# Kernel tuning notes

Hardware: AMD Instinct MI355X
Metric: run time of the kernel (lower is better)

Reference implementation:

```python
import jax, jax.numpy as jnp
import numpy as np

B, S, H = 2, 2048, 2048
INTER = 1024
N_ROUTED = 8
ZERO = 4
TOTAL = N_ROUTED + ZERO
TOP_K = 2
SCALE = 1.5


def setup_inputs() -> dict:
    key = jax.random.key(0)
    k0, k1, k2, k3, k4, k5 = jax.random.split(key, 6)
    w = 0.02  # weight init scale
    return {
        "hidden_states": jax.random.normal(k0, (B, S, H), jnp.float32),
        "classifier_w": jax.random.normal(k1, (TOTAL, H), jnp.float32) * w,
        "e_score_correction_bias": jax.random.normal(k2, (TOTAL,), jnp.float32) * w,
        "gate_w": jax.random.normal(k3, (N_ROUTED, INTER, H), jnp.float32) * w,
        "up_w": jax.random.normal(k4, (N_ROUTED, INTER, H), jnp.float32) * w,
        "down_w": jax.random.normal(k5, (N_ROUTED, H, INTER), jnp.float32) * w,
    }


def reference(hidden_states, classifier_w, e_score_correction_bias, gate_w, up_w, down_w):
    x = hidden_states  # [B,S,H]
    total = classifier_w.shape[0]
    n_routed = gate_w.shape[0]

    # --- Router: softmax over all experts, bias only for selection ---
    logits = jnp.einsum('bsh,eh->bse', x, classifier_w)          # [B,S,total]
    probs = jax.nn.softmax(logits, axis=-1)
    biased = probs + e_score_correction_bias
    _, idx = jax.lax.top_k(biased, TOP_K)                         # [B,S,K] int
    rw = jnp.take_along_axis(probs, idx, axis=-1) * SCALE         # unbiased probs as weights

    # Dense per-expert weight via one-hot combine (Equal+Mul+ReduceSum in original)
    w_full = jnp.sum(jax.nn.one_hot(idx, total, dtype=x.dtype) * rw[..., None], axis=-2)  # [B,S,total]

    # --- Compute ALL routed experts densely (matches original op graph) ---
    g = jnp.einsum('bsh,eih->bsei', x, gate_w)                    # [B,S,E,INTER]
    u = jnp.einsum('bsh,eih->bsei', x, up_w)
    act = jax.nn.silu(g) * u
    expert_out = jnp.einsum('bsei,ehi->bseh', act, down_w)        # [B,S,E,H]

    out = jnp.einsum('bse,bseh->bsh', w_full[..., :n_routed], expert_out)
    # Zero (identity) experts pass hidden_states through
    out = out + x * jnp.sum(w_full[..., n_routed:], axis=-1, keepdims=True)
    return out
```

## Files before the change

kernel.cpp:

```cpp
#include <hip/hip_runtime.h>
#include <cstdint>

#define T_TOKENS 4096
#define HDIM 2048
#define IDIM 1024
#define NEXP 8
#define NTOT 12
#define MAX_SLOTS 8320

typedef __bf16 bf16x8_t __attribute__((ext_vector_type(8)));
typedef float f32x4_t __attribute__((ext_vector_type(4)));
typedef unsigned short u16x8_t __attribute__((ext_vector_type(8)));
typedef unsigned short u16x4_t __attribute__((ext_vector_type(4)));

__device__ __forceinline__ unsigned short f2bf(float f) {
    unsigned int u = __builtin_bit_cast(unsigned int, f);
    u += 0x7fffu + ((u >> 16) & 1u);
    return (unsigned short)(u >> 16);
}
__device__ __forceinline__ float bfu2f(unsigned short u) {
    unsigned int v = ((unsigned int)u) << 16;
    return __builtin_bit_cast(float, v);
}
__device__ __forceinline__ void async16(const unsigned short* g, unsigned short* l) {
    __builtin_amdgcn_global_load_lds(
        (const unsigned int __attribute__((address_space(1)))*)g,
        (unsigned int __attribute__((address_space(3)))*)l,
        16, 0, 0);
}
__device__ __forceinline__ void cvt16(const float* src, unsigned short* dst) {
    f32x4_t f0 = ((const f32x4_t*)src)[0];
    f32x4_t f1 = ((const f32x4_t*)src)[1];
    f32x4_t f2 = ((const f32x4_t*)src)[2];
    f32x4_t f3 = ((const f32x4_t*)src)[3];
    u16x8_t a, b;
#pragma unroll
    for (int j = 0; j < 4; ++j) { a[j] = f2bf(f0[j]); a[4 + j] = f2bf(f1[j]); }
#pragma unroll
    for (int j = 0; j < 4; ++j) { b[j] = f2bf(f2[j]); b[4 + j] = f2bf(f3[j]); }
    ((u16x8_t*)dst)[0] = a;
    ((u16x8_t*)dst)[1] = b;
}

__global__ void init_kernel(int* __restrict__ meta) {
    int i = threadIdx.x;
    if (i < 32) meta[i] = 0;
}

__global__ void noop_kernel() {}

__global__ void pack_w_kernel(const float* __restrict__ gw, const float* __restrict__ uw,
                              const float* __restrict__ dw,
                              unsigned short* __restrict__ guwb,
                              unsigned short* __restrict__ dwb) {
    const int n8_gu = NEXP * 2 * IDIM * HDIM / 8;
    const int n8_d = NEXP * HDIM * IDIM / 8;
    int stride = gridDim.x * blockDim.x;
    for (int i = blockIdx.x * blockDim.x + threadIdx.x; i < n8_gu + n8_d; i += stride) {
        if (i < n8_gu) {
            size_t f = (size_t)i * 8;
            int h = (int)(f & (HDIM - 1));
            int p = (int)((f >> 11) & 2047);
            int e = (int)(f >> 22);
            int j = p >> 5, r = p & 31;
            const float* base = (r < 16) ? gw : uw;
            const float* src = base + ((size_t)e * IDIM + 16 * j + (r & 15)) * HDIM + h;
            f32x4_t a = ((const f32x4_t*)src)[0];
            f32x4_t b = ((const f32x4_t*)src)[1];
            u16x8_t o;
#pragma unroll
            for (int q = 0; q < 4; ++q) { o[q] = f2bf(a[q]); o[4 + q] = f2bf(b[q]); }
            ((u16x8_t*)guwb)[i] = o;
        } else {
            int k = i - n8_gu;
            const f32x4_t* p4 = (const f32x4_t*)(dw + (size_t)k * 8);
            f32x4_t a = p4[0], b = p4[1];
            u16x8_t o;
#pragma unroll
            for (int q = 0; q < 4; ++q) { o[q] = f2bf(a[q]); o[4 + q] = f2bf(b[q]); }
            ((u16x8_t*)dwb)[k] = o;
        }
    }
}

__global__ void router_kernel(const float* __restrict__ x,
                              const float* __restrict__ cw,
                              const float* __restrict__ bias,
                              int* __restrict__ counts,
                              int* __restrict__ tok_e,
                              float* __restrict__ tok_w,
                              float* __restrict__ zero_w,
                              unsigned short* __restrict__ xb) {
    const int token = blockIdx.x;
    const int ln = threadIdx.x;
    const float* xr = x + (size_t)token * HDIM;
    float acc[NTOT];
#pragma unroll
    for (int e = 0; e < NTOT; ++e) acc[e] = 0.f;
    for (int h0 = ln * 4; h0 < HDIM; h0 += 256) {
        f32x4_t xv = *(const f32x4_t*)(xr + h0);
        if (xb) {
            u16x4_t o;
#pragma unroll
            for (int j = 0; j < 4; ++j) o[j] = f2bf(xv[j]);
            *(u16x4_t*)(xb + (size_t)token * HDIM + h0) = o;
        }
#pragma unroll
        for (int e = 0; e < NTOT; ++e) {
            f32x4_t wv = *(const f32x4_t*)(cw + e * HDIM + h0);
            acc[e] += xv[0] * wv[0] + xv[1] * wv[1] + xv[2] * wv[2] + xv[3] * wv[3];
        }
    }
#pragma unroll
    for (int e = 0; e < NTOT; ++e) {
        float v = acc[e];
#pragma unroll
        for (int s = 32; s > 0; s >>= 1) v += __shfl_xor(v, s, 64);
        acc[e] = v;
    }
    if (ln == 0) {
        float mx = acc[0];
#pragma unroll
        for (int e = 1; e < NTOT; ++e) mx = fmaxf(mx, acc[e]);
        float p[NTOT];
        float sum = 0.f;
#pragma unroll
        for (int e = 0; e < NTOT; ++e) { p[e] = __expf(acc[e] - mx); sum += p[e]; }
        float inv = 1.f / sum;
#pragma unroll
        for (int e = 0; e < NTOT; ++e) p[e] *= inv;
        float b[NTOT];
#pragma unroll
        for (int e = 0; e < NTOT; ++e) b[e] = p[e] + bias[e];
        int i0 = 0; float v0 = b[0];
#pragma unroll
        for (int e = 1; e < NTOT; ++e) if (b[e] > v0) { v0 = b[e]; i0 = e; }
        int i1 = -1; float v1 = -3.0e38f;
#pragma unroll
        for (int e = 0; e < NTOT; ++e) if (e != i0 && b[e] > v1) { v1 = b[e]; i1 = e; }
        if (i1 < 0) i1 = (i0 == 0) ? 1 : 0;
        float w0 = p[i0] * 1.5f, w1 = p[i1] * 1.5f;
        tok_e[2 * token] = i0; tok_e[2 * token + 1] = i1;
        tok_w[2 * token] = w0; tok_w[2 * token + 1] = w1;
        float zw = 0.f;
        if (i0 >= NEXP) zw += w0; else atomicAdd(&counts[i0], 1);
        if (i1 >= NEXP) zw += w1; else atomicAdd(&counts[i1], 1);
        zero_w[token] = zw;
    }
}

__global__ void scan_kernel(const int* __restrict__ counts, int* __restrict__ offs) {
    if (threadIdx.x == 0 && blockIdx.x == 0) {
        int a = 0;
        for (int e = 0; e < NEXP; ++e) {
            offs[e] = a;
            int c = counts[e];
            if (c < 0) c = 0;
            if (c > T_TOKENS) c = T_TOKENS;
            a += c;
        }
        if (a > 2 * T_TOKENS) a = 2 * T_TOKENS;
        offs[NEXP] = a;
    }
}

__global__ void place_kernel(const int* __restrict__ tok_e, const float* __restrict__ tok_w,
                             const int* __restrict__ offs, int* __restrict__ fill,
                             int* __restrict__ token_list, float* __restrict__ slot_w,
                             int* __restrict__ map) {
    int token = blockIdx.x * blockDim.x + threadIdx.x;
    if (token >= T_TOKENS) return;
#pragma unroll
    for (int j = 0; j < 2; ++j) {
        int e = tok_e[2 * token + j];
        int m = -1;
        if (e >= 0 && e < NEXP) {
            int pos = atomicAdd(&fill[e], 1);
            int slot = offs[e] + pos;
            if (slot >= 0 && slot < 2 * T_TOKENS) {
                token_list[slot] = token;
                slot_w[slot] = tok_w[2 * token + j];
                m = slot;
            }
        }
        map[2 * token + j] = m;
    }
}

__launch_bounds__(256, 3)
__global__ void gemm1_kernel(const unsigned short* __restrict__ xb,
                             const unsigned short* __restrict__ guwb,
                             const int* __restrict__ offs,
                             const int* __restrict__ token_list,
                             const float* __restrict__ slot_w,
                             unsigned short* __restrict__ act) {
    const int e = blockIdx.z;
    const int off = offs[e];
    int Me = offs[e + 1] - off;
    if (Me < 0) Me = 0;
    if (Me > T_TOKENS) Me = T_TOKENS;
    const int m0 = blockIdx.y * 128;
    if (m0 >= Me) return;
    const int n0 = blockIdx.x * 128;

    __shared__ __align__(16) unsigned short As[128][32];
    __shared__ __align__(16) unsigned short Bs[128][32];

    const int tid = threadIdx.x;
    const int wv = tid >> 6, ln = tid & 63;
    const int sc = (ln & 3) * 8;

    int tr0 = m0 + wv * 16 + (ln >> 2);      if (tr0 >= Me) tr0 = Me - 1;
    int tr1 = m0 + 64 + wv * 16 + (ln >> 2); if (tr1 >= Me) tr1 = Me - 1;
    int tok0 = token_list[off + tr0]; if (tok0 < 0 || tok0 >= T_TOKENS) tok0 = 0;
    int tok1 = token_list[off + tr1]; if (tok1 < 0 || tok1 >= T_TOKENS) tok1 = 0;
    const unsigned short* aA0 = xb + (size_t)tok0 * HDIM + sc;
    const unsigned short* aA1 = xb + (size_t)tok1 * HDIM + sc;
    unsigned short* lA0 = &As[wv * 16][0];
    unsigned short* lA1 = &As[64 + wv * 16][0];

    const unsigned short* aB0 = guwb + (size_t)e * 2 * IDIM * HDIM +
                                (size_t)(n0 + wv * 16 + (ln >> 2)) * HDIM + sc;
    const unsigned short* aB1 = aB0 + (size_t)64 * HDIM;
    unsigned short* lB0 = &Bs[wv * 16][0];
    unsigned short* lB1 = &Bs[64 + wv * 16][0];

    const int wm = wv & 1, wn = wv >> 1;
    const int fr = ln & 15;
    const int fk = (ln >> 4) * 8;

    f32x4_t acc[4][4] = {};

    for (int k0 = 0; k0 < HDIM; k0 += 32) {
        async16(aA0 + k0, lA0);
        async16(aA1 + k0, lA1);
        async16(aB0 + k0, lB0);
        async16(aB1 + k0, lB1);
        __syncthreads();
        bf16x8_t af[4], bfr[4];
#pragma unroll
        for (int t = 0; t < 4; ++t) {
            af[t] = *(const bf16x8_t*)&As[wm * 64 + t * 16 + fr][fk];
            bfr[t] = *(const bf16x8_t*)&Bs[wn * 64 + t * 16 + fr][fk];
        }
#pragma unroll
        for (int mt = 0; mt < 4; ++mt)
#pragma unroll
            for (int nt = 0; nt < 4; ++nt)
                acc[mt][nt] = __builtin_amdgcn_mfma_f32_16x16x32_bf16(af[mt], bfr[nt], acc[mt][nt], 0, 0, 0);
        __syncthreads();
    }

    const int ibase = (n0 >> 1) + wn * 32;
#pragma unroll
    for (int mt = 0; mt < 4; ++mt) {
#pragma unroll
        for (int r = 0; r < 4; ++r) {
            int rloc = wm * 64 + mt * 16 + (ln >> 4) * 4 + r;
            int grow = m0 + rloc;
            if (grow < Me) {
                float w = slot_w[off + grow];
                size_t rb = (size_t)(off + grow) * IDIM + ibase;
#pragma unroll
                for (int t = 0; t < 2; ++t) {
                    float g = acc[mt][2 * t][r];
                    float u = acc[mt][2 * t + 1][r];
                    float s = g / (1.f + __expf(-g));
                    act[rb + t * 16 + fr] = f2bf(s * u * w);
                }
            }
        }
    }
}

__launch_bounds__(256, 3)
__global__ void gemm2_kernel(const unsigned short* __restrict__ act,
                             const unsigned short* __restrict__ dwb,
                             const int* __restrict__ offs,
                             unsigned short* __restrict__ dout) {
    const int e = blockIdx.z;
    const int off = offs[e];
    int Me = offs[e + 1] - off;
    if (Me < 0) Me = 0;
    if (Me > T_TOKENS) Me = T_TOKENS;
    const int m0 = blockIdx.y * 128;
    if (m0 >= Me) return;
    const int n0 = blockIdx.x * 128;

    __shared__ __align__(16) unsigned short As[128][32];
    __shared__ __align__(16) unsigned short Bs[128][32];

    const int tid = threadIdx.x;
    const int wv = tid >> 6, ln = tid & 63;
    const int sc = (ln & 3) * 8;

    const int sr = wv * 16 + (ln >> 2);
    int ar0 = off + m0 + sr;      if (ar0 >= MAX_SLOTS) ar0 = MAX_SLOTS - 1;
    int ar1 = off + m0 + 64 + sr; if (ar1 >= MAX_SLOTS) ar1 = MAX_SLOTS - 1;
    const unsigned short* aA0 = act + (size_t)ar0 * IDIM + sc;
    const unsigned short* aA1 = act + (size_t)ar1 * IDIM + sc;
    unsigned short* lA0 = &As[wv * 16][0];
    unsigned short* lA1 = &As[64 + wv * 16][0];

    const unsigned short* aB0 = dwb + (size_t)e * HDIM * IDIM +
                                (size_t)(n0 + wv * 16 + (ln >> 2)) * IDIM + sc;
    const unsigned short* aB1 = aB0 + (size_t)64 * IDIM;
    unsigned short* lB0 = &Bs[wv * 16][0];
    unsigned short* lB1 = &Bs[64 + wv * 16][0];

    const int wm = wv & 1, wn = wv >> 1;
    const int fr = ln & 15;
    const int fk = (ln >> 4) * 8;

    f32x4_t acc[4][4] = {};

    for (int k0 = 0; k0 < IDIM; k0 += 32) {
        async16(aA0 + k0, lA0);
        async16(aA1 + k0, lA1);
        async16(aB0 + k0, lB0);
        async16(aB1 + k0, lB1);
        __syncthreads();
        bf16x8_t af[4], bfr[4];
#pragma unroll
        for (int t = 0; t < 4; ++t) {
            af[t] = *(const bf16x8_t*)&As[wm * 64 + t * 16 + fr][fk];
            bfr[t] = *(const bf16x8_t*)&Bs[wn * 64 + t * 16 + fr][fk];
        }
#pragma unroll
        for (int mt = 0; mt < 4; ++mt)
#pragma unroll
            for (int nt = 0; nt < 4; ++nt)
                acc[mt][nt] = __builtin_amdgcn_mfma_f32_16x16x32_bf16(af[mt], bfr[nt], acc[mt][nt], 0, 0, 0);
        __syncthreads();
    }

#pragma unroll
    for (int mt = 0; mt < 4; ++mt) {
#pragma unroll
        for (int r = 0; r < 4; ++r) {
            int rloc = wm * 64 + mt * 16 + (ln >> 4) * 4 + r;
            int grow = m0 + rloc;
            if (grow < Me) {
                size_t rb = (size_t)(off + grow) * HDIM + n0;
#pragma unroll
                for (int nt = 0; nt < 4; ++nt)
                    dout[rb + wn * 64 + nt * 16 + fr] = f2bf(acc[mt][nt][r]);
            }
        }
    }
}

__launch_bounds__(256, 2)
__global__ void gemm1_fb(const float* __restrict__ x,
                         const float* __restrict__ gate_w,
                         const float* __restrict__ up_w,
                         const int* __restrict__ offs,
                         const int* __restrict__ token_list,
                         const float* __restrict__ slot_w,
                         unsigned short* __restrict__ act) {
    const int e = blockIdx.z;
    const int off = offs[e];
    int Me = offs[e + 1] - off;
    if (Me < 0) Me = 0;
    if (Me > T_TOKENS) Me = T_TOKENS;
    const int m0 = blockIdx.y * 128;
    if (m0 >= Me) return;
    const int n0 = blockIdx.x * 128;

    __shared__ __align__(16) unsigned short As[128][32];
    __shared__ __align__(16) unsigned short Gs[128][32];
    __shared__ __align__(16) unsigned short Us[128][32];

    const int tid = threadIdx.x;
    const int srow = tid >> 1;
    const int shalf = (tid & 1) * 16;

    int tr = m0 + srow; if (tr >= Me) tr = Me - 1;
    int tok = token_list[off + tr];
    if (tok < 0 || tok >= T_TOKENS) tok = 0;
    const float* aA = x + (size_t)tok * HDIM + shalf;
    const float* aG = gate_w + (size_t)e * IDIM * HDIM + (size_t)(n0 + srow) * HDIM + shalf;
    const float* aU = up_w + (size_t)e * IDIM * HDIM + (size_t)(n0 + srow) * HDIM + shalf;
    unsigned short* lA = &As[srow][shalf];
    unsigned short* lG = &Gs[srow][shalf];
    unsigned short* lU = &Us[srow][shalf];

    const int wv = tid >> 6, ln = tid & 63;
    const int wm = wv & 1, wn = wv >> 1;
    const int fr = ln & 15;
    const int fk = (ln >> 4) * 8;

    f32x4_t accg[4][4] = {};
    f32x4_t accu[4][4] = {};

    for (int k0 = 0; k0 < HDIM; k0 += 32) {
        cvt16(aA + k0, lA);
        cvt16(aG + k0, lG);
        cvt16(aU + k0, lU);
        __syncthreads();
        bf16x8_t af[4], gf[4], uf[4];
#pragma unroll
        for (int t = 0; t < 4; ++t) {
            af[t] = *(const bf16x8_t*)&As[wm * 64 + t * 16 + fr][fk];
            gf[t] = *(const bf16x8_t*)&Gs[wn * 64 + t * 16 + fr][fk];
            uf[t] = *(const bf16x8_t*)&Us[wn * 64 + t * 16 + fr][fk];
        }
#pragma unroll
        for (int mt = 0; mt < 4; ++mt)
#pragma unroll
            for (int nt = 0; nt < 4; ++nt) {
                accg[mt][nt] = __builtin_amdgcn_mfma_f32_16x16x32_bf16(af[mt], gf[nt], accg[mt][nt], 0, 0, 0);
                accu[mt][nt] = __builtin_amdgcn_mfma_f32_16x16x32_bf16(af[mt], uf[nt], accu[mt][nt], 0, 0, 0);
            }
        __syncthreads();
    }

#pragma unroll
    for (int mt = 0; mt < 4; ++mt) {
#pragma unroll
        for (int r = 0; r < 4; ++r) {
            int rloc = wm * 64 + mt * 16 + (ln >> 4) * 4 + r;
            int grow = m0 + rloc;
            if (grow < Me) {
                float w = slot_w[off + grow];
                size_t rb = (size_t)(off + grow) * IDIM + n0;
#pragma unroll
                for (int nt = 0; nt < 4; ++nt) {
                    float g = accg[mt][nt][r];
                    float u = accu[mt][nt][r];
                    float s = g / (1.f + __expf(-g));
                    act[rb + wn * 64 + nt * 16 + fr] = f2bf(s * u * w);
                }
            }
        }
    }
}

__launch_bounds__(256, 2)
__global__ void gemm2_fb(const unsigned short* __restrict__ act,
                         const float* __restrict__ dwn,
                         const int* __restrict__ offs,
                         unsigned short* __restrict__ dout) {
    const int e = blockIdx.z;
    const int off = offs[e];
    int Me = offs[e + 1] - off;
    if (Me < 0) Me = 0;
    if (Me > T_TOKENS) Me = T_TOKENS;
    const int m0 = blockIdx.y * 128;
    if (m0 >= Me) return;
    const int n0 = blockIdx.x * 128;

    __shared__ __align__(16) unsigned short As[128][32];
    __shared__ __align__(16) unsigned short Bs[128][32];

    const int tid = threadIdx.x;
    const int wv = tid >> 6, ln = tid & 63;

    const int sr0 = wv * 16 + (ln >> 2);
    const int sc = (ln & 3) * 8;
    int ar0 = off + m0 + sr0;      if (ar0 >= MAX_SLOTS) ar0 = MAX_SLOTS - 1;
    int ar1 = off + m0 + 64 + sr0; if (ar1 >= MAX_SLOTS) ar1 = MAX_SLOTS - 1;
    const unsigned short* aA0 = act + (size_t)ar0 * IDIM + sc;
    const unsigned short* aA1 = act + (size_t)ar1 * IDIM + sc;
    unsigned short* lA0 = &As[wv * 16][0];
    unsigned short* lA1 = &As[64 + wv * 16][0];

    const int srow = tid >> 1;
    const int shalf = (tid & 1) * 16;
    const float* aB = dwn + (size_t)e * HDIM * IDIM + (size_t)(n0 + srow) * IDIM + shalf;
    unsigned short* lB = &Bs[srow][shalf];

    const int wm = wv & 1, wn = wv >> 1;
    const int fr = ln & 15;
    const int fk = (ln >> 4) * 8;

    f32x4_t acc[4][4] = {};

    for (int k0 = 0; k0 < IDIM; k0 += 32) {
        async16(aA0 + k0, lA0);
        async16(aA1 + k0, lA1);
        cvt16(aB + k0, lB);
        __syncthreads();
        bf16x8_t af[4], bfr[4];
#pragma unroll
        for (int t = 0; t < 4; ++t) {
            af[t] = *(const bf16x8_t*)&As[wm * 64 + t * 16 + fr][fk];
            bfr[t] = *(const bf16x8_t*)&Bs[wn * 64 + t * 16 + fr][fk];
        }
#pragma unroll
        for (int mt = 0; mt < 4; ++mt)
#pragma unroll
            for (int nt = 0; nt < 4; ++nt)
                acc[mt][nt] = __builtin_amdgcn_mfma_f32_16x16x32_bf16(af[mt], bfr[nt], acc[mt][nt], 0, 0, 0);
        __syncthreads();
    }

#pragma unroll
    for (int mt = 0; mt < 4; ++mt) {
#pragma unroll
        for (int r = 0; r < 4; ++r) {
            int rloc = wm * 64 + mt * 16 + (ln >> 4) * 4 + r;
            int grow = m0 + rloc;
            if (grow < Me) {
                size_t rb = (size_t)(off + grow) * HDIM + n0;
#pragma unroll
                for (int nt = 0; nt < 4; ++nt)
                    dout[rb + wn * 64 + nt * 16 + fr] = f2bf(acc[mt][nt][r]);
            }
        }
    }
}

__global__ void finalize_kernel(const float* __restrict__ x,
                                const unsigned short* __restrict__ dout,
                                const int* __restrict__ map,
                                const float* __restrict__ zero_w,
                                float* __restrict__ out) {
    int gid = blockIdx.x * blockDim.x + threadIdx.x;
    int token = gid >> 8;
    int hg = (gid & 255) * 8;
    int s0 = map[2 * token], s1 = map[2 * token + 1];
    float zw = zero_w[token];
    size_t base = (size_t)token * HDIM + hg;
    f32x4_t x0 = *(const f32x4_t*)(x + base);
    f32x4_t x1 = *(const f32x4_t*)(x + base + 4);
    float o[8];
#pragma unroll
    for (int j = 0; j < 4; ++j) { o[j] = zw * x0[j]; o[4 + j] = zw * x1[j]; }
    if (s0 >= 0 && s0 < 2 * T_TOKENS) {
        u16x8_t d = *(const u16x8_t*)(dout + (size_t)s0 * HDIM + hg);
#pragma unroll
        for (int j = 0; j < 8; ++j) o[j] += bfu2f(d[j]);
    }
    if (s1 >= 0 && s1 < 2 * T_TOKENS) {
        u16x8_t d = *(const u16x8_t*)(dout + (size_t)s1 * HDIM + hg);
#pragma unroll
        for (int j = 0; j < 8; ++j) o[j] += bfu2f(d[j]);
    }
    f32x4_t o0, o1;
#pragma unroll
    for (int j = 0; j < 4; ++j) { o0[j] = o[j]; o1[j] = o[4 + j]; }
    *(f32x4_t*)(out + base) = o0;
    *(f32x4_t*)(out + base + 4) = o1;
}

extern "C" void kernel_launch(void* const* d_in, const int* in_sizes, int n_in,
                              void* d_out, int out_size, void* d_ws, size_t ws_size,
                              hipStream_t stream) {
    const float* x = (const float*)d_in[0];
    const float* cw = (const float*)d_in[1];
    const float* bias = (const float*)d_in[2];
    const float* gw = (const float*)d_in[3];
    const float* uw = (const float*)d_in[4];
    const float* dw = (const float*)d_in[5];
    float* out = (float*)d_out;

    char* ws = (char*)d_ws;
    int* counts = (int*)(ws + 0);
    int* fill = (int*)(ws + 32);
    int* offs = (int*)(ws + 64);
    int* tok_e = (int*)(ws + 128);
    float* tok_w = (float*)(ws + 32896);
    float* zero_w = (float*)(ws + 65664);
    int* map = (int*)(ws + 82048);
    int* token_list = (int*)(ws + 114816);
    float* slot_w = (float*)(ws + 148096);
    unsigned short* act = (unsigned short*)(ws + 181504);
    unsigned short* dout = (unsigned short*)(ws + 17220864);
    const size_t needed_small = 51299584ull;
    unsigned short* xb   = (unsigned short*)(ws + 51299584ull);
    unsigned short* guwb = (unsigned short*)(ws + 68076800ull);
    unsigned short* dwb  = (unsigned short*)(ws + 135185664ull);
    const size_t needed_big = 168740096ull;

    if (ws_size < needed_small) {
        noop_kernel<<<1, 64, 0, stream>>>();
        return;
    }

    init_kernel<<<1, 64, 0, stream>>>((int*)ws);

    if (ws_size >= needed_big) {
        router_kernel<<<T_TOKENS, 64, 0, stream>>>(x, cw, bias, counts, tok_e, tok_w, zero_w, xb);
        scan_kernel<<<1, 64, 0, stream>>>(counts, offs);
        place_kernel<<<(T_TOKENS + 255) / 256, 256, 0, stream>>>(tok_e, tok_w, offs, fill,
                                                                 token_list, slot_w, map);
        pack_w_kernel<<<4096, 256, 0, stream>>>(gw, uw, dw, guwb, dwb);
        gemm1_kernel<<<dim3(2 * IDIM / 128, 32, NEXP), 256, 0, stream>>>(xb, guwb, offs,
                                                                         token_list, slot_w, act);
        gemm2_kernel<<<dim3(HDIM / 128, 32, NEXP), 256, 0, stream>>>(act, dwb, offs, dout);
    } else {
        router_kernel<<<T_TOKENS, 64, 0, stream>>>(x, cw, bias, counts, tok_e, tok_w, zero_w,
                                                   (unsigned short*)nullptr);
        scan_kernel<<<1, 64, 0, stream>>>(counts, offs);
        place_kernel<<<(T_TOKENS + 255) / 256, 256, 0, stream>>>(tok_e, tok_w, offs, fill,
                                                                 token_list, slot_w, map);
        gemm1_fb<<<dim3(IDIM / 128, 32, NEXP), 256, 0, stream>>>(x, gw, uw, offs,
                                                                 token_list, slot_w, act);
        gemm2_fb<<<dim3(HDIM / 128, 32, NEXP), 256, 0, stream>>>(act, dw, offs, dout);
    }

    finalize_kernel<<<(T_TOKENS * HDIM / 8 + 255) / 256, 256, 0, stream>>>(x, dout, map,
                                                                           zero_w, out);
}
```

Before: 500.4 us.

## Double-buffer LDS tiles and XOR-swizzle columns in both expert GEMMs

Both grouped GEMM kernels now use two LDS buffers, so the next K-slice is loaded asynchronously while MFMAs run on the current one, which hides global-load latency behind compute. The global source column is XOR-swizzled per row and the fragment read column is swizzled to match, with the aim of reducing LDS bank conflicts on the 16-byte fragment reads. LDS use doubles, which may lower occupancy under launch_bounds(256,3). The single barrier per iteration relies on the async-load wait semantics being correct for the prefetched buffer.

Result: no change. 501.1 us (+0.1%).

```diff
diff --git a/kernel.cpp b/kernel.cpp
--- a/kernel.cpp
+++ b/kernel.cpp
@@ -203,45 +203,53 @@
     if (m0 >= Me) return;
     const int n0 = blockIdx.x * 128;
 
-    __shared__ __align__(16) unsigned short As[128][32];
-    __shared__ __align__(16) unsigned short Bs[128][32];
+    __shared__ __align__(16) unsigned short As[2][128][32];
+    __shared__ __align__(16) unsigned short Bs[2][128][32];
 
     const int tid = threadIdx.x;
     const int wv = tid >> 6, ln = tid & 63;
-    const int sc = (ln & 3) * 8;
-
-    int tr0 = m0 + wv * 16 + (ln >> 2);      if (tr0 >= Me) tr0 = Me - 1;
-    int tr1 = m0 + 64 + wv * 16 + (ln >> 2); if (tr1 >= Me) tr1 = Me - 1;
+    const int R = ln >> 2;
+    const int scs = (((ln & 3) ^ ((R & 3) ^ ((R >> 2) & 1))) * 8);
+
+    int tr0 = m0 + wv * 16 + R;      if (tr0 >= Me) tr0 = Me - 1;
+    int tr1 = m0 + 64 + wv * 16 + R; if (tr1 >= Me) tr1 = Me - 1;
     int tok0 = token_list[off + tr0]; if (tok0 < 0 || tok0 >= T_TOKENS) tok0 = 0;
     int tok1 = token_list[off + tr1]; if (tok1 < 0 || tok1 >= T_TOKENS) tok1 = 0;
-    const unsigned short* aA0 = xb + (size_t)tok0 * HDIM + sc;
-    const unsigned short* aA1 = xb + (size_t)tok1 * HDIM + sc;
-    unsigned short* lA0 = &As[wv * 16][0];
-    unsigned short* lA1 = &As[64 + wv * 16][0];
+    const unsigned short* aA0 = xb + (size_t)tok0 * HDIM + scs;
+    const unsigned short* aA1 = xb + (size_t)tok1 * HDIM + scs;
 
     const unsigned short* aB0 = guwb + (size_t)e * 2 * IDIM * HDIM +
-                                (size_t)(n0 + wv * 16 + (ln >> 2)) * HDIM + sc;
+                                (size_t)(n0 + wv * 16 + R) * HDIM + scs;
     const unsigned short* aB1 = aB0 + (size_t)64 * HDIM;
-    unsigned short* lB0 = &Bs[wv * 16][0];
-    unsigned short* lB1 = &Bs[64 + wv * 16][0];
 
     const int wm = wv & 1, wn = wv >> 1;
     const int fr = ln & 15;
     const int fk = (ln >> 4) * 8;
+    const int fswz = ((fr & 3) ^ ((fr >> 2) & 1)) * 8;
+    const int fcol = fk ^ fswz;
 
     f32x4_t acc[4][4] = {};
 
+    async16(aA0, &As[0][wv * 16][0]);
+    async16(aA1, &As[0][64 + wv * 16][0]);
+    async16(aB0, &Bs[0][wv * 16][0]);
+    async16(aB1, &Bs[0][64 + wv * 16][0]);
+    __syncthreads();
+
+    int cur = 0;
     for (int k0 = 0; k0 < HDIM; k0 += 32) {
-        async16(aA0 + k0, lA0);
-        async16(aA1 + k0, lA1);
-        async16(aB0 + k0, lB0);
-        async16(aB1 + k0, lB1);
-        __syncthreads();
+        const int nxt = cur ^ 1;
+        if (k0 + 32 < HDIM) {
+            async16(aA0 + k0 + 32, &As[nxt][wv * 16][0]);
+            async16(aA1 + k0 + 32, &As[nxt][64 + wv * 16][0]);
+            async16(aB0 + k0 + 32, &Bs[nxt][wv * 16][0]);
+            async16(aB1 + k0 + 32, &Bs[nxt][64 + wv * 16][0]);
+        }
         bf16x8_t af[4], bfr[4];
 #pragma unroll
         for (int t = 0; t < 4; ++t) {
-            af[t] = *(const bf16x8_t*)&As[wm * 64 + t * 16 + fr][fk];
-            bfr[t] = *(const bf16x8_t*)&Bs[wn * 64 + t * 16 + fr][fk];
+            af[t] = *(const bf16x8_t*)&As[cur][wm * 64 + t * 16 + fr][fcol];
+            bfr[t] = *(const bf16x8_t*)&Bs[cur][wn * 64 + t * 16 + fr][fcol];
         }
 #pragma unroll
         for (int mt = 0; mt < 4; ++mt)
@@ -249,6 +257,7 @@
             for (int nt = 0; nt < 4; ++nt)
                 acc[mt][nt] = __builtin_amdgcn_mfma_f32_16x16x32_bf16(af[mt], bfr[nt], acc[mt][nt], 0, 0, 0);
         __syncthreads();
+        cur = nxt;
     }
 
     const int ibase = (n0 >> 1) + wn * 32;
@@ -287,44 +296,51 @@
     if (m0 >= Me) return;
     const int n0 = blockIdx.x * 128;
 
-    __shared__ __align__(16) unsigned short As[128][32];
-    __shared__ __align__(16) unsigned short Bs[128][32];
+    __shared__ __align__(16) unsigned short As[2][128][32];
+    __shared__ __align__(16) unsigned short Bs[2][128][32];
 
     const int tid = threadIdx.x;
     const int wv = tid >> 6, ln = tid & 63;
-    const int sc = (ln & 3) * 8;
-
-    const int sr = wv * 16 + (ln >> 2);
-    int ar0 = off + m0 + sr;      if (ar0 >= MAX_SLOTS) ar0 = MAX_SLOTS - 1;
-    int ar1 = off + m0 + 64 + sr; if (ar1 >= MAX_SLOTS) ar1 = MAX_SLOTS - 1;
-    const unsigned short* aA0 = act + (size_t)ar0 * IDIM + sc;
-    const unsigned short* aA1 = act + (size_t)ar1 * IDIM + sc;
-    unsigned short* lA0 = &As[wv * 16][0];
-    unsigned short* lA1 = &As[64 + wv * 16][0];
+    const int R = ln >> 2;
+    const int scs = (((ln & 3) ^ ((R & 3) ^ ((R >> 2) & 1))) * 8);
+
+    int ar0 = off + m0 + wv * 16 + R;      if (ar0 >= MAX_SLOTS) ar0 = MAX_SLOTS - 1;
+    int ar1 = off + m0 + 64 + wv * 16 + R; if (ar1 >= MAX_SLOTS) ar1 = MAX_SLOTS - 1;
+    const unsigned short* aA0 = act + (size_t)ar0 * IDIM + scs;
+    const unsigned short* aA1 = act + (size_t)ar1 * IDIM + scs;
 
     const unsigned short* aB0 = dwb + (size_t)e * HDIM * IDIM +
-                                (size_t)(n0 + wv * 16 + (ln >> 2)) * IDIM + sc;
+                                (size_t)(n0 + wv * 16 + R) * IDIM + scs;
     const unsigned short* aB1 = aB0 + (size_t)64 * IDIM;
-    unsigned short* lB0 = &Bs[wv * 16][0];
-    unsigned short* lB1 = &Bs[64 + wv * 16][0];
 
     const int wm = wv & 1, wn = wv >> 1;
     const int fr = ln & 15;
     const int fk = (ln >> 4) * 8;
+    const int fswz = ((fr & 3) ^ ((fr >> 2) & 1)) * 8;
+    const int fcol = fk ^ fswz;
 
     f32x4_t acc[4][4] = {};
 
+    async16(aA0, &As[0][wv * 16][0]);
+    async16(aA1, &As[0][64 + wv * 16][0]);
+    async16(aB0, &Bs[0][wv * 16][0]);
+    async16(aB1, &Bs[0][64 + wv * 16][0]);
+    __syncthreads();
+
+    int cur = 0;
     for (int k0 = 0; k0 < IDIM; k0 += 32) {
-        async16(aA0 + k0, lA0);
-        async16(aA1 + k0, lA1);
-        async16(aB0 + k0, lB0);
-        async16(aB1 + k0, lB1);
-        __syncthreads();
+        const int nxt = cur ^ 1;
+        if (k0 + 32 < IDIM) {
+            async16(aA0 + k0 + 32, &As[nxt][wv * 16][0]);
+            async16(aA1 + k0 + 32, &As[nxt][64 + wv * 16][0]);
+            async16(aB0 + k0 + 32, &Bs[nxt][wv * 16][0]);
+            async16(aB1 + k0 + 32, &Bs[nxt][64 + wv * 16][0]);
+        }
         bf16x8_t af[4], bfr[4];
 #pragma unroll
         for (int t = 0; t < 4; ++t) {
-            af[t] = *(const bf16x8_t*)&As[wm * 64 + t * 16 + fr][fk];
-            bfr[t] = *(const bf16x8_t*)&Bs[wn * 64 + t * 16 + fr][fk];
+            af[t] = *(const bf16x8_t*)&As[cur][wm * 64 + t * 16 + fr][fcol];
+            bfr[t] = *(const bf16x8_t*)&Bs[cur][wn * 64 + t * 16 + fr][fcol];
         }
 #pragma unroll
         for (int mt = 0; mt < 4; ++mt)
@@ -332,6 +348,7 @@
             for (int nt = 0; nt < 4; ++nt)
                 acc[mt][nt] = __builtin_amdgcn_mfma_f32_16x16x32_bf16(af[mt], bfr[nt], acc[mt][nt], 0, 0, 0);
         __syncthreads();
+        cur = nxt;
     }
 
 #pragma unroll
```

## Triple-buffer LDS pipeline and widen expert GEMM tiles to 128x256 with 512 threads

Applied to the files above, without the earlier changes.

Both expert GEMM kernels now use a 3-stage software pipeline of asynchronous global-to-LDS loads. Explicit vmcnt waits and raw barriers replace the two __syncthreads per k-step, and MFMA runs at raised priority. The block tile grows from 128x128 to 128x256 using 8 waves, so each block reuses more of its loaded data per k-step and the grid is halved. In exchange, LDS use per block rises to about 72KB, which limits how many blocks fit on a CU, and correctness depends on the hand-counted vmcnt values.

Measured after the change: 522.4 us. +4.4%, slower.

```diff
diff --git a/kernel.cpp b/kernel.cpp
--- a/kernel.cpp
+++ b/kernel.cpp
@@ -12,6 +12,9 @@
 typedef float f32x4_t __attribute__((ext_vector_type(4)));
 typedef unsigned short u16x8_t __attribute__((ext_vector_type(8)));
 typedef unsigned short u16x4_t __attribute__((ext_vector_type(4)));
+
+#define WAITV(N) asm volatile("s_waitcnt vmcnt(" #N ")" ::: "memory")
+#define CFENCE asm volatile("" ::: "memory")
 
 __device__ __forceinline__ unsigned short f2bf(float f) {
     unsigned int u = __builtin_bit_cast(unsigned int, f);
@@ -187,7 +190,7 @@
     }
 }
 
-__launch_bounds__(256, 3)
+__launch_bounds__(512, 4)
 __global__ void gemm1_kernel(const unsigned short* __restrict__ xb,
                              const unsigned short* __restrict__ guwb,
                              const int* __restrict__ offs,
@@ -201,29 +204,25 @@
     if (Me > T_TOKENS) Me = T_TOKENS;
     const int m0 = blockIdx.y * 128;
     if (m0 >= Me) return;
-    const int n0 = blockIdx.x * 128;
-
-    __shared__ __align__(16) unsigned short As[128][32];
-    __shared__ __align__(16) unsigned short Bs[128][32];
+    const int n0 = blockIdx.x * 256;
+
+    __shared__ __align__(16) unsigned short As[3][128][32];
+    __shared__ __align__(16) unsigned short Bs[3][256][32];
 
     const int tid = threadIdx.x;
     const int wv = tid >> 6, ln = tid & 63;
     const int sc = (ln & 3) * 8;
-
-    int tr0 = m0 + wv * 16 + (ln >> 2);      if (tr0 >= Me) tr0 = Me - 1;
-    int tr1 = m0 + 64 + wv * 16 + (ln >> 2); if (tr1 >= Me) tr1 = Me - 1;
-    int tok0 = token_list[off + tr0]; if (tok0 < 0 || tok0 >= T_TOKENS) tok0 = 0;
-    int tok1 = token_list[off + tr1]; if (tok1 < 0 || tok1 >= T_TOKENS) tok1 = 0;
-    const unsigned short* aA0 = xb + (size_t)tok0 * HDIM + sc;
-    const unsigned short* aA1 = xb + (size_t)tok1 * HDIM + sc;
-    unsigned short* lA0 = &As[wv * 16][0];
-    unsigned short* lA1 = &As[64 + wv * 16][0];
+    const int srow = ln >> 2;
+
+    int tr = m0 + wv * 16 + srow;
+    if (tr >= Me) tr = Me - 1;
+    int tok = token_list[off + tr];
+    if (tok < 0 || tok >= T_TOKENS) tok = 0;
+    const unsigned short* aA = xb + (size_t)tok * HDIM + sc;
 
     const unsigned short* aB0 = guwb + (size_t)e * 2 * IDIM * HDIM +
-                                (size_t)(n0 + wv * 16 + (ln >> 2)) * HDIM + sc;
-    const unsigned short* aB1 = aB0 + (size_t)64 * HDIM;
-    unsigned short* lB0 = &Bs[wv * 16][0];
-    unsigned short* lB1 = &Bs[64 + wv * 16][0];
+                                (size_t)(n0 + wv * 16 + srow) * HDIM + sc;
+    const unsigned short* aB1 = aB0 + (size_t)128 * HDIM;
 
     const int wm = wv & 1, wn = wv >> 1;
     const int fr = ln & 15;
@@ -231,25 +230,54 @@
 
     f32x4_t acc[4][4] = {};
 
-    for (int k0 = 0; k0 < HDIM; k0 += 32) {
-        async16(aA0 + k0, lA0);
-        async16(aA1 + k0, lA1);
-        async16(aB0 + k0, lB0);
-        async16(aB1 + k0, lB1);
-        __syncthreads();
+    auto STAGE = [&](int kt, int b) {
+        const int k0 = kt * 32;
+        async16(aA + k0, &As[b][wv * 16][0]);
+        async16(aB0 + k0, &Bs[b][wv * 16][0]);
+        async16(aB1 + k0, &Bs[b][128 + wv * 16][0]);
+    };
+    auto COMPUTE = [&](int b) {
         bf16x8_t af[4], bfr[4];
 #pragma unroll
         for (int t = 0; t < 4; ++t) {
-            af[t] = *(const bf16x8_t*)&As[wm * 64 + t * 16 + fr][fk];
-            bfr[t] = *(const bf16x8_t*)&Bs[wn * 64 + t * 16 + fr][fk];
-        }
+            af[t] = *(const bf16x8_t*)&As[b][wm * 64 + t * 16 + fr][fk];
+            bfr[t] = *(const bf16x8_t*)&Bs[b][wn * 64 + t * 16 + fr][fk];
+        }
+        __builtin_amdgcn_s_setprio(1);
 #pragma unroll
         for (int mt = 0; mt < 4; ++mt)
 #pragma unroll
             for (int nt = 0; nt < 4; ++nt)
                 acc[mt][nt] = __builtin_amdgcn_mfma_f32_16x16x32_bf16(af[mt], bfr[nt], acc[mt][nt], 0, 0, 0);
-        __syncthreads();
-    }
+        __builtin_amdgcn_s_setprio(0);
+    };
+
+    const int NT = HDIM / 32;
+    STAGE(0, 0);
+    STAGE(1, 1);
+    int cur = 0, nb = 2;
+    for (int t = 0; t < NT - 2; ++t) {
+        STAGE(t + 2, nb);
+        WAITV(6);
+        __builtin_amdgcn_s_barrier();
+        CFENCE;
+        COMPUTE(cur);
+        CFENCE;
+        __builtin_amdgcn_s_barrier();
+        if (++cur == 3) cur = 0;
+        if (++nb == 3) nb = 0;
+    }
+    WAITV(3);
+    __builtin_amdgcn_s_barrier();
+    CFENCE;
+    COMPUTE(cur);
+    CFENCE;
+    __builtin_amdgcn_s_barrier();
+    if (++cur == 3) cur = 0;
+    WAITV(0);
+    __builtin_amdgcn_s_barrier();
+    CFENCE;
+    COMPUTE(cur);
 
     const int ibase = (n0 >> 1) + wn * 32;
 #pragma unroll
@@ -273,7 +301,7 @@
     }
 }
 
-__launch_bounds__(256, 3)
+__launch_bounds__(512, 4)
 __global__ void gemm2_kernel(const unsigned short* __restrict__ act,
                              const unsigned short* __restrict__ dwb,
                              const int* __restrict__ offs,
@@ -285,28 +313,23 @@
     if (Me > T_TOKENS) Me = T_TOKENS;
     const int m0 = blockIdx.y * 128;
     if (m0 >= Me) return;
-    const int n0 = blockIdx.x * 128;
-
-    __shared__ __align__(16) unsigned short As[128][32];
-    __shared__ __align__(16) unsigned short Bs[128][32];
+    const int n0 = blockIdx.x * 256;
+
+    __shared__ __align__(16) unsigned short As[3][128][32];
+    __shared__ __align__(16) unsigned short Bs[3][256][32];
 
     const int tid = threadIdx.x;
     const int wv = tid >> 6, ln = tid & 63;
     const int sc = (ln & 3) * 8;
-
-    const int sr = wv * 16 + (ln >> 2);
-    int ar0 = off + m0 + sr;      if (ar0 >= MAX_SLOTS) ar0 = MAX_SLOTS - 1;
-    int ar1 = off + m0 + 64 + sr; if (ar1 >= MAX_SLOTS) ar1 = MAX_SLOTS - 1;
-    const unsigned short* aA0 = act + (size_t)ar0 * IDIM + sc;
-    const unsigned short* aA1 = act + (size_t)ar1 * IDIM + sc;
-    unsigned short* lA0 = &As[wv * 16][0];
-    unsigned short* lA1 = &As[64 + wv * 16][0];
+    const int srow = ln >> 2;
+
+    int ar = off + m0 + wv * 16 + srow;
+    if (ar >= MAX_SLOTS) ar = MAX_SLOTS - 1;
+    const unsigned short* aA = act + (size_t)ar * IDIM + sc;
 
     const unsigned short* aB0 = dwb + (size_t)e * HDIM * IDIM +
-                                (size_t)(n0 + wv * 16 + (ln >> 2)) * IDIM + sc;
-    const unsigned short* aB1 = aB0 + (size_t)64 * IDIM;
-    unsigned short* lB0 = &Bs[wv * 16][0];
-    unsigned short* lB1 = &Bs[64 + wv * 16][0];
+                                (size_t)(n0 + wv * 16 + srow) * IDIM + sc;
+    const unsigned short* aB1 = aB0 + (size_t)128 * IDIM;
 
     const int wm = wv & 1, wn = wv >> 1;
     const int fr = ln & 15;
@@ -314,25 +337,54 @@
 
     f32x4_t acc[4][4] = {};
 
-    for (int k0 = 0; k0 < IDIM; k0 += 32) {
-        async16(aA0 + k0, lA0);
-        async16(aA1 + k0, lA1);
-        async16(aB0 + k0, lB0);
-        async16(aB1 + k0, lB1);
-        __syncthreads();
+    auto STAGE = [&](int kt, int b) {
+        const int k0 = kt * 32;
+        async16(aA + k0, &As[b][wv * 16][0]);
+        async16(aB0 + k0, &Bs[b][wv * 16][0]);
+        async16(aB1 + k0, &Bs[b][128 + wv * 16][0]);
+    };
+    auto COMPUTE = [&](int b) {
         bf16x8_t af[4], bfr[4];
 #pragma unroll
         for (int t = 0; t < 4; ++t) {
-            af[t] = *(const bf16x8_t*)&As[wm * 64 + t * 16 + fr][fk];
-            bfr[t] = *(const bf16x8_t*)&Bs[wn * 64 + t * 16 + fr][fk];
-        }
+            af[t] = *(const bf16x8_t*)&As[b][wm * 64 + t * 16 + fr][fk];
+            bfr[t] = *(const bf16x8_t*)&Bs[b][wn * 64 + t * 16 + fr][fk];
+        }
+        __builtin_amdgcn_s_setprio(1);
 #pragma unroll
         for (int mt = 0; mt < 4; ++mt)
 #pragma unroll
             for (int nt = 0; nt < 4; ++nt)
                 acc[mt][nt] = __builtin_amdgcn_mfma_f32_16x16x32_bf16(af[mt], bfr[nt], acc[mt][nt], 0, 0, 0);
-        __syncthreads();
-    }
+        __builtin_amdgcn_s_setprio(0);
+    };
+
+    const int NT = IDIM / 32;
+    STAGE(0, 0);
+    STAGE(1, 1);
+    int cur = 0, nb = 2;
+    for (int t = 0; t < NT - 2; ++t) {
+        STAGE(t + 2, nb);
+        WAITV(6);
+        __builtin_amdgcn_s_barrier();
+        CFENCE;
+        COMPUTE(cur);
+        CFENCE;
+        __builtin_amdgcn_s_barrier();
+        if (++cur == 3) cur = 0;
+        if (++nb == 3) nb = 0;
+    }
+    WAITV(3);
+    __builtin_amdgcn_s_barrier();
+    CFENCE;
+    COMPUTE(cur);
+    CFENCE;
+    __builtin_amdgcn_s_barrier();
+    if (++cur == 3) cur = 0;
+    WAITV(0);
+    __builtin_amdgcn_s_barrier();
+    CFENCE;
+    COMPUTE(cur);
 
 #pragma unroll
     for (int mt = 0; mt < 4; ++mt) {
@@ -586,9 +638,9 @@
         place_kernel<<<(T_TOKENS + 255) / 256, 256, 0, stream>>>(tok_e, tok_w, offs, fill,
                                                                  token_list, slot_w, map);
         pack_w_kernel<<<4096, 256, 0, stream>>>(gw, uw, dw, guwb, dwb);
-        gemm1_kernel<<<dim3(2 * IDIM / 128, 32, NEXP), 256, 0, stream>>>(xb, guwb, offs,
+        gemm1_kernel<<<dim3(2 * IDIM / 256, 32, NEXP), 512, 0, stream>>>(xb, guwb, offs,
                                                                          token_list, slot_w, act);
-        gemm2_kernel<<<dim3(HDIM / 128, 32, NEXP), 256, 0, stream>>>(act, dwb, offs, dout);
+        gemm2_kernel<<<dim3(HDIM / 256, 32, NEXP), 512, 0, stream>>>(act, dwb, offs, dout);
     } else {
         router_kernel<<<T_TOKENS, 64, 0, stream>>>(x, cw, bias, counts, tok_e, tok_w, zero_w,
                                                    (unsigned short*)nullptr);
```

## Scatter gemm2 results into output with atomics and drop finalize pass

Applied to the files above, without the earlier changes.

The down-projection GEMM now atomically adds its fp32 results straight into the output rows of each routed token, after a new kernel fills the output with the zero-expert identity term. This removes the bf16 intermediate dout buffer and the separate finalize kernel. The weight-packing kernel is replaced by a plain per-tensor bf16 conversion, and gemm1 picks gate or up rows by wave from separate buffers instead of an interleaved layout. In exchange it adds float atomics on the output, which are nondeterministic and contend when a token's two experts write the same row, and it shrinks the workspace footprint.

After: 519.2 us. 1.04x slower.

```diff
diff --git a/kernel.cpp b/kernel.cpp
--- a/kernel.cpp
+++ b/kernel.cpp
@@ -49,37 +49,23 @@
 
 __global__ void noop_kernel() {}
 
-__global__ void pack_w_kernel(const float* __restrict__ gw, const float* __restrict__ uw,
-                              const float* __restrict__ dw,
-                              unsigned short* __restrict__ guwb,
-                              unsigned short* __restrict__ dwb) {
-    const int n8_gu = NEXP * 2 * IDIM * HDIM / 8;
-    const int n8_d = NEXP * HDIM * IDIM / 8;
+__global__ void cvt3_kernel(const float* __restrict__ gw, const float* __restrict__ uw,
+                            const float* __restrict__ dw,
+                            unsigned short* __restrict__ gwb, unsigned short* __restrict__ uwb,
+                            unsigned short* __restrict__ dwb) {
+    const int n8 = 3 * (1 << 21);
     int stride = gridDim.x * blockDim.x;
-    for (int i = blockIdx.x * blockDim.x + threadIdx.x; i < n8_gu + n8_d; i += stride) {
-        if (i < n8_gu) {
-            size_t f = (size_t)i * 8;
-            int h = (int)(f & (HDIM - 1));
-            int p = (int)((f >> 11) & 2047);
-            int e = (int)(f >> 22);
-            int j = p >> 5, r = p & 31;
-            const float* base = (r < 16) ? gw : uw;
-            const float* src = base + ((size_t)e * IDIM + 16 * j + (r & 15)) * HDIM + h;
-            f32x4_t a = ((const f32x4_t*)src)[0];
-            f32x4_t b = ((const f32x4_t*)src)[1];
-            u16x8_t o;
-#pragma unroll
-            for (int q = 0; q < 4; ++q) { o[q] = f2bf(a[q]); o[4 + q] = f2bf(b[q]); }
-            ((u16x8_t*)guwb)[i] = o;
-        } else {
-            int k = i - n8_gu;
-            const f32x4_t* p4 = (const f32x4_t*)(dw + (size_t)k * 8);
-            f32x4_t a = p4[0], b = p4[1];
-            u16x8_t o;
-#pragma unroll
-            for (int q = 0; q < 4; ++q) { o[q] = f2bf(a[q]); o[4 + q] = f2bf(b[q]); }
-            ((u16x8_t*)dwb)[k] = o;
-        }
+    for (int i = blockIdx.x * blockDim.x + threadIdx.x; i < n8; i += stride) {
+        int seg = i >> 21;
+        int k = i & ((1 << 21) - 1);
+        const float* s = (seg == 0) ? gw : (seg == 1) ? uw : dw;
+        unsigned short* d = (seg == 0) ? gwb : (seg == 1) ? uwb : dwb;
+        const f32x4_t* p = (const f32x4_t*)(s + (size_t)k * 8);
+        f32x4_t a = p[0], b = p[1];
+        u16x8_t o;
+#pragma unroll
+        for (int j = 0; j < 4; ++j) { o[j] = f2bf(a[j]); o[4 + j] = f2bf(b[j]); }
+        ((u16x8_t*)d)[k] = o;
     }
 }
 
@@ -187,9 +173,26 @@
     }
 }
 
+__global__ void preout_kernel(const float* __restrict__ x, const float* __restrict__ zero_w,
+                              float* __restrict__ out) {
+    int gid = blockIdx.x * blockDim.x + threadIdx.x;
+    int token = gid >> 8;
+    int hg = (gid & 255) * 8;
+    float zw = zero_w[token];
+    size_t base = (size_t)token * HDIM + hg;
+    f32x4_t x0 = *(const f32x4_t*)(x + base);
+    f32x4_t x1 = *(const f32x4_t*)(x + base + 4);
+    f32x4_t o0, o1;
+#pragma unroll
+    for (int j = 0; j < 4; ++j) { o0[j] = zw * x0[j]; o1[j] = zw * x1[j]; }
+    *(f32x4_t*)(out + base) = o0;
+    *(f32x4_t*)(out + base + 4) = o1;
+}
+
 __launch_bounds__(256, 3)
 __global__ void gemm1_kernel(const unsigned short* __restrict__ xb,
-                             const unsigned short* __restrict__ guwb,
+                             const unsigned short* __restrict__ gwb,
+                             const unsigned short* __restrict__ uwb,
                              const int* __restrict__ offs,
                              const int* __restrict__ token_list,
                              const float* __restrict__ slot_w,
@@ -209,9 +212,10 @@
     const int tid = threadIdx.x;
     const int wv = tid >> 6, ln = tid & 63;
     const int sc = (ln & 3) * 8;
-
-    int tr0 = m0 + wv * 16 + (ln >> 2);      if (tr0 >= Me) tr0 = Me - 1;
-    int tr1 = m0 + 64 + wv * 16 + (ln >> 2); if (tr1 >= Me) tr1 = Me - 1;
+    const int R = ln >> 2;
+
+    int tr0 = m0 + wv * 16 + R;      if (tr0 >= Me) tr0 = Me - 1;
+    int tr1 = m0 + 64 + wv * 16 + R; if (tr1 >= Me) tr1 = Me - 1;
     int tok0 = token_list[off + tr0]; if (tok0 < 0 || tok0 >= T_TOKENS) tok0 = 0;
     int tok1 = token_list[off + tr1]; if (tok1 < 0 || tok1 >= T_TOKENS) tok1 = 0;
     const unsigned short* aA0 = xb + (size_t)tok0 * HDIM + sc;
@@ -219,9 +223,10 @@
     unsigned short* lA0 = &As[wv * 16][0];
     unsigned short* lA1 = &As[64 + wv * 16][0];
 
-    const unsigned short* aB0 = guwb + (size_t)e * 2 * IDIM * HDIM +
-                                (size_t)(n0 + wv * 16 + (ln >> 2)) * HDIM + sc;
-    const unsigned short* aB1 = aB0 + (size_t)64 * HDIM;
+    const unsigned short* wsel = (wv & 1) ? uwb : gwb;
+    const unsigned short* aB0 = wsel + (size_t)e * IDIM * HDIM +
+                                (size_t)((n0 >> 1) + (wv >> 1) * 16 + R) * HDIM + sc;
+    const unsigned short* aB1 = aB0 + (size_t)32 * HDIM;
     unsigned short* lB0 = &Bs[wv * 16][0];
     unsigned short* lB1 = &Bs[64 + wv * 16][0];
 
@@ -277,7 +282,8 @@
 __global__ void gemm2_kernel(const unsigned short* __restrict__ act,
                              const unsigned short* __restrict__ dwb,
                              const int* __restrict__ offs,
-                             unsigned short* __restrict__ dout) {
+                             const int* __restrict__ token_list,
+                             float* __restrict__ out) {
     const int e = blockIdx.z;
     const int off = offs[e];
     int Me = offs[e + 1] - off;
@@ -293,17 +299,17 @@
     const int tid = threadIdx.x;
     const int wv = tid >> 6, ln = tid & 63;
     const int sc = (ln & 3) * 8;
-
-    const int sr = wv * 16 + (ln >> 2);
-    int ar0 = off + m0 + sr;      if (ar0 >= MAX_SLOTS) ar0 = MAX_SLOTS - 1;
-    int ar1 = off + m0 + 64 + sr; if (ar1 >= MAX_SLOTS) ar1 = MAX_SLOTS - 1;
+    const int R = ln >> 2;
+
+    int ar0 = off + m0 + wv * 16 + R;      if (ar0 >= MAX_SLOTS) ar0 = MAX_SLOTS - 1;
+    int ar1 = off + m0 + 64 + wv * 16 + R; if (ar1 >= MAX_SLOTS) ar1 = MAX_SLOTS - 1;
     const unsigned short* aA0 = act + (size_t)ar0 * IDIM + sc;
     const unsigned short* aA1 = act + (size_t)ar1 * IDIM + sc;
     unsigned short* lA0 = &As[wv * 16][0];
     unsigned short* lA1 = &As[64 + wv * 16][0];
 
     const unsigned short* aB0 = dwb + (size_t)e * HDIM * IDIM +
-                                (size_t)(n0 + wv * 16 + (ln >> 2)) * IDIM + sc;
+                                (size_t)(n0 + wv * 16 + R) * IDIM + sc;
     const unsigned short* aB1 = aB0 + (size_t)64 * IDIM;
     unsigned short* lB0 = &Bs[wv * 16][0];
     unsigned short* lB1 = &Bs[64 + wv * 16][0];
@@ -341,10 +347,13 @@
             int rloc = wm * 64 + mt * 16 + (ln >> 4) * 4 + r;
             int grow = m0 + rloc;
             if (grow < Me) {
-                size_t rb = (size_t)(off + grow) * HDIM + n0;
-#pragma unroll
-                for (int nt = 0; nt < 4; ++nt)
-                    dout[rb + wn * 64 + nt * 16 + fr] = f2bf(acc[mt][nt][r]);
+                int tokr = token_list[off + grow];
+                if (tokr >= 0 && tokr < T_TOKENS) {
+                    size_t rb = (size_t)tokr * HDIM + n0;
+#pragma unroll
+                    for (int nt = 0; nt < 4; ++nt)
+                        atomicAdd(&out[rb + wn * 64 + nt * 16 + fr], acc[mt][nt][r]);
+                }
             }
         }
     }
@@ -568,10 +577,11 @@
     unsigned short* act = (unsigned short*)(ws + 181504);
     unsigned short* dout = (unsigned short*)(ws + 17220864);
     const size_t needed_small = 51299584ull;
-    unsigned short* xb   = (unsigned short*)(ws + 51299584ull);
-    unsigned short* guwb = (unsigned short*)(ws + 68076800ull);
-    unsigned short* dwb  = (unsigned short*)(ws + 135185664ull);
-    const size_t needed_big = 168740096ull;
+    unsigned short* xb  = (unsigned short*)(ws + 17220864ull);
+    unsigned short* gwb = (unsigned short*)(ws + 33998080ull);
+    unsigned short* uwb = (unsigned short*)(ws + 67552512ull);
+    unsigned short* dwb = (unsigned short*)(ws + 101106944ull);
+    const size_t needed_big = 134661376ull;
 
     if (ws_size < needed_small) {
         noop_kernel<<<1, 64, 0, stream>>>();
@@ -585,10 +595,12 @@
         scan_kernel<<<1, 64, 0, stream>>>(counts, offs);
         place_kernel<<<(T_TOKENS + 255) / 256, 256, 0, stream>>>(tok_e, tok_w, offs, fill,
                                                                  token_list, slot_w, map);
-        pack_w_kernel<<<4096, 256, 0, stream>>>(gw, uw, dw, guwb, dwb);
-        gemm1_kernel<<<dim3(2 * IDIM / 128, 32, NEXP), 256, 0, stream>>>(xb, guwb, offs,
+        cvt3_kernel<<<4096, 256, 0, stream>>>(gw, uw, dw, gwb, uwb, dwb);
+        preout_kernel<<<T_TOKENS, 256, 0, stream>>>(x, zero_w, out);
+        gemm1_kernel<<<dim3(2 * IDIM / 128, 32, NEXP), 256, 0, stream>>>(xb, gwb, uwb, offs,
                                                                          token_list, slot_w, act);
-        gemm2_kernel<<<dim3(HDIM / 128, 32, NEXP), 256, 0, stream>>>(act, dwb, offs, dout);
+        gemm2_kernel<<<dim3(HDIM / 128, 32, NEXP), 256, 0, stream>>>(act, dwb, offs,
+                                                                     token_list, out);
     } else {
         router_kernel<<<T_TOKENS, 64, 0, stream>>>(x, cw, bias, counts, tok_e, tok_w, zero_w,
                                                    (unsigned short*)nullptr);
@@ -598,8 +610,7 @@
         gemm1_fb<<<dim3(IDIM / 128, 32, NEXP), 256, 0, stream>>>(x, gw, uw, offs,
                                                                  token_list, slot_w, act);
         gemm2_fb<<<dim3(HDIM / 128, 32, NEXP), 256, 0, stream>>>(act, dw, offs, dout);
-    }
-
-    finalize_kernel<<<(T_TOKENS * HDIM / 8 + 255) / 256, 256, 0, stream>>>(x, dout, map,
-                                                                           zero_w, out);
-}
+        finalize_kernel<<<(T_TOKENS * HDIM / 8 + 255) / 256, 256, 0, stream>>>(x, dout, map,
+                                                                               zero_w, out);
+    }
+}
```
